# Optimization experiments

Measured on AMD Instinct MI355X. Metric: run time of the kernel, lower is better.

Reference implementation:

```python
import jax, jax.numpy as jnp
import numpy as np

B, C, H, W = 16, 64, 1024, 16  # requires C*W == H per the module's implicit view/matmul constraint
C8 = C // 8


def setup_inputs() -> dict:
    key = jax.random.key(0)
    ks = jax.random.split(key, 7)
    s_in = 1.0 / np.sqrt(C)
    return {
        "x": jax.random.normal(ks[0], (B, C, H, W), dtype=jnp.float32),
        "Wq": jax.random.normal(ks[1], (C8, C), dtype=jnp.float32) * s_in,
        "bq": jax.random.normal(ks[2], (C8,), dtype=jnp.float32) * 0.01,
        "Wk": jax.random.normal(ks[3], (C8, C), dtype=jnp.float32) * s_in,
        "bk": jax.random.normal(ks[4], (C8,), dtype=jnp.float32) * 0.01,
        "Wv": jax.random.normal(ks[5], (C, C), dtype=jnp.float32) * s_in,
        "bv": jax.random.normal(ks[6], (C,), dtype=jnp.float32) * 0.01,
    }


def conv1x1(x, w, b):
    # 1x1 conv == per-pixel channel mixing: [B,C,H,W] x [O,C] -> [B,O,H,W]
    return jnp.einsum("bchw,oc->bohw", x, w) + b[None, :, None, None]


def reference(x, Wq, bq, Wk, bk, Wv, bv):
    b, c, h, w = x.shape
    q = conv1x1(x, Wq, bq)  # [B, C/8, H, W]
    k = conv1x1(x, Wk, bk)  # [B, C/8, H, W]
    v = conv1x1(x, Wv, bv)  # [B, C, H, W]
    # Faithful to torch .view(B, -1, H): row-major reshape, NOT a transpose.
    qf = jnp.swapaxes(q.reshape(b, -1, h), 1, 2)  # [B, H, C8*W]
    kf = k.reshape(b, -1, h)                      # [B, C8*W, H]
    vf = v.reshape(b, -1, h)                      # [B, C*W, H] (C*W == H)
    scores = jax.nn.softmax(jnp.matmul(qf, kf), axis=-1)  # [B, H, H]
    attended = jnp.matmul(scores, vf)             # [B, H, H]
    attended = attended.reshape(v.shape)          # [B, C, H, W]
    return x + attended
```

## Files before the change

### kernel.cpp

```cpp
#include <hip/hip_runtime.h>
#include <stdint.h>

typedef uint32_t u32;
typedef __attribute__((ext_vector_type(4))) float f32x4;
typedef __attribute__((ext_vector_type(8))) short short8;

#define NBATCH 16
#define NPIX   16384
#define NPB    1048576

__device__ __forceinline__ ushort f2bf(float f) {
  u32 b = __builtin_bit_cast(u32, f);
  return (ushort)((b + 0x7FFFu + ((b >> 16) & 1u)) >> 16);
}
__device__ __forceinline__ float bf2f(ushort h) {
  return __builtin_bit_cast(float, (u32)h << 16);
}

__device__ __forceinline__ void gload16(const void* g, void* l) {
  __builtin_amdgcn_global_load_lds(
      (const __attribute__((address_space(1))) u32*)g,
      (__attribute__((address_space(3))) u32*)l,
      16, 0, 0);
}

__global__ void prep_w2(const float* __restrict__ Wq, const float* __restrict__ bq,
                        const float* __restrict__ Wk, const float* __restrict__ bk,
                        const float* __restrict__ Wv, const float* __restrict__ bv,
                        ushort* __restrict__ Wpk, float* __restrict__ bpk)
{
  int gid = blockIdx.x * 256 + threadIdx.x;
  if (gid < 12288) {
    int m = gid >> 7, kk = gid & 127;
    int ch = kk & 63;
    ushort outv = 0;
    if (m < 8) {
      float wv = Wq[m * 64 + ch];
      ushort h = f2bf(wv);
      outv = (kk < 64) ? h : f2bf(wv - bf2f(h));
    } else if (m < 16) {
      float wv = Wk[(m - 8) * 64 + ch];
      ushort h = f2bf(wv);
      outv = (kk < 64) ? h : f2bf(wv - bf2f(h));
    } else if (m < 80) {
      outv = (kk < 64) ? f2bf(Wv[(m - 16) * 64 + ch]) : (ushort)0;
    }
    Wpk[gid] = outv;
  } else if (gid < 12368) {
    int o = gid - 12288;
    bpk[o] = (o < 8) ? bq[o] : (o < 16 ? bk[o - 8] : bv[o - 16]);
  }
}

__global__ __launch_bounds__(256) void proj10(
    const float* __restrict__ x, const ushort* __restrict__ Wpk,
    const float* __restrict__ bpk,
    ushort* __restrict__ Qt2, ushort* __restrict__ Kt2,
    ushort* __restrict__ Vt)
{
  __shared__ __align__(16) char smem[32768];
  float* xs = (float*)smem;
  int t = threadIdx.x;
  int w = t >> 6, lane = t & 63;
  int l15 = lane & 15, l4 = lane >> 4;

  int g = blockIdx.x;
  int lin = (g & 7) * 256 + (g >> 3);
  int b = lin >> 7;
  int l0 = (lin & 127) << 3;
  const float* xb = x + (size_t)b * NPB + l0;

  #pragma unroll
  for (int it = 0; it < 8; ++it) {
    int f0 = (it * 4 + w) * 64;
    int f = f0 + lane;
    int ch = f >> 5, r2 = f & 31, tc = r2 >> 1, half = r2 & 1;
    gload16(xb + (size_t)ch * NPIX + tc * 1024 + half * 4, xs + f0 * 4);
  }

  const uint4* Wp4 = (const uint4*)Wpk;
  uint4 Afrag[12];
  #pragma unroll
  for (int kc = 0; kc < 4; ++kc)
    Afrag[kc] = Wp4[l15 * 16 + kc * 4 + l4];
  #pragma unroll
  for (int mt = 1; mt < 5; ++mt)
    #pragma unroll
    for (int kc = 0; kc < 2; ++kc)
      Afrag[2 + mt * 2 + kc] = Wp4[(mt * 16 + l15) * 16 + kc * 4 + l4];

  f32x4 acc[5][2];
  #pragma unroll
  for (int mt = 0; mt < 5; ++mt) {
    f32x4 bv4;
    #pragma unroll
    for (int r = 0; r < 4; ++r) bv4[r] = bpk[mt * 16 + l4 * 4 + r];
    acc[mt][0] = bv4; acc[mt][1] = bv4;
  }

  __syncthreads();

  #pragma unroll
  for (int i = 0; i < 2; ++i) {
    int px = (w * 2 + i) * 16 + l15;
    u32 xr[16];
    #pragma unroll
    for (int kc = 0; kc < 2; ++kc)
      #pragma unroll
      for (int j = 0; j < 8; ++j)
        xr[kc * 8 + j] = ((const u32*)xs)[(kc * 32 + l4 * 8 + j) * 128 + px];
    uint4 bxh[2], bxl[2];
    #pragma unroll
    for (int kc = 0; kc < 2; ++kc)
      #pragma unroll
      for (int p = 0; p < 4; ++p) {
        u32 a = xr[kc * 8 + 2 * p], c = xr[kc * 8 + 2 * p + 1];
        ((u32*)&bxh[kc])[p] = (a >> 16) | (c & 0xFFFF0000u);
        float fa = __builtin_bit_cast(float, a) -
                   __builtin_bit_cast(float, a & 0xFFFF0000u);
        float fc = __builtin_bit_cast(float, c) -
                   __builtin_bit_cast(float, c & 0xFFFF0000u);
        u32 la = __builtin_bit_cast(u32, fa), lc = __builtin_bit_cast(u32, fc);
        ((u32*)&bxl[kc])[p] = (la >> 16) | (lc & 0xFFFF0000u);
      }
    short8 h0 = __builtin_bit_cast(short8, bxh[0]);
    short8 h1 = __builtin_bit_cast(short8, bxh[1]);
    short8 s0 = __builtin_bit_cast(short8, bxl[0]);
    short8 s1 = __builtin_bit_cast(short8, bxl[1]);
    acc[0][i] = __builtin_amdgcn_mfma_f32_16x16x32_bf16(
        __builtin_bit_cast(short8, Afrag[0]), h0, acc[0][i], 0, 0, 0);
    acc[0][i] = __builtin_amdgcn_mfma_f32_16x16x32_bf16(
        __builtin_bit_cast(short8, Afrag[1]), h1, acc[0][i], 0, 0, 0);
    acc[0][i] = __builtin_amdgcn_mfma_f32_16x16x32_bf16(
        __builtin_bit_cast(short8, Afrag[0]), s0, acc[0][i], 0, 0, 0);
    acc[0][i] = __builtin_amdgcn_mfma_f32_16x16x32_bf16(
        __builtin_bit_cast(short8, Afrag[1]), s1, acc[0][i], 0, 0, 0);
    acc[0][i] = __builtin_amdgcn_mfma_f32_16x16x32_bf16(
        __builtin_bit_cast(short8, Afrag[2]), h0, acc[0][i], 0, 0, 0);
    acc[0][i] = __builtin_amdgcn_mfma_f32_16x16x32_bf16(
        __builtin_bit_cast(short8, Afrag[3]), h1, acc[0][i], 0, 0, 0);
    #pragma unroll
    for (int mt = 1; mt < 5; ++mt) {
      acc[mt][i] = __builtin_amdgcn_mfma_f32_16x16x32_bf16(
          __builtin_bit_cast(short8, Afrag[2 + mt * 2]), h0, acc[mt][i], 0, 0, 0);
      acc[mt][i] = __builtin_amdgcn_mfma_f32_16x16x32_bf16(
          __builtin_bit_cast(short8, Afrag[3 + mt * 2]), h1, acc[mt][i], 0, 0, 0);
    }
  }
  __syncthreads();

  float*  qkl = (float*)smem;
  ushort* vl  = (ushort*)(smem + 16 * 132 * 4);
  #pragma unroll
  for (int i = 0; i < 2; ++i) {
    int px = (w * 2 + i) * 16 + l15;
    #pragma unroll
    for (int r = 0; r < 4; ++r)
      qkl[(l4 * 4 + r) * 132 + px] = acc[0][i][r];
    #pragma unroll
    for (int mt = 1; mt < 5; ++mt)
      #pragma unroll
      for (int r = 0; r < 4; ++r)
        vl[((mt - 1) * 16 + l4 * 4 + r) * 136 + px] = f2bf(acc[mt][i][r]);
  }
  __syncthreads();

  if (t < 128) {
    int l = t >> 4, tcc = t & 15;
    size_t lrow = (size_t)b * 1024 + l0 + l;
    int px = tcc * 8 + l;

    union { ushort s[8]; uint4 v; } qh, ql, kh, kl;
    #pragma unroll
    for (int o = 0; o < 8; ++o) {
      float qv = qkl[o * 132 + px];
      ushort h = f2bf(qv);
      qh.s[o] = h; ql.s[o] = f2bf(qv - bf2f(h));
      float kv = qkl[(8 + o) * 132 + px];
      h = f2bf(kv);
      kh.s[o] = h; kl.s[o] = f2bf(kv - bf2f(h));
    }
    ushort* qrow = Qt2 + lrow * 384 + tcc * 8;
    *(uint4*)qrow         = qh.v;
    *(uint4*)(qrow + 128) = ql.v;
    *(uint4*)(qrow + 256) = qh.v;
    ushort* krow = Kt2 + lrow * 384 + tcc * 8;
    *(uint4*)krow         = kh.v;
    *(uint4*)(krow + 128) = kh.v;
    *(uint4*)(krow + 256) = kl.v;

    ushort* vrow = Vt + lrow * 1024;
    #pragma unroll
    for (int it = 0; it < 4; ++it) {
      int c2 = (it << 4) + tcc;
      union { ushort s[16]; uint4 q[2]; } ov;
      #pragma unroll
      for (int tt = 0; tt < 16; ++tt)
        ov.s[tt] = vl[c2 * 136 + tt * 8 + l];
      *(uint4*)(vrow + c2 * 16)     = ov.q[0];
      *(uint4*)(vrow + c2 * 16 + 8) = ov.q[1];
    }
  }
}

template<int KTOT, bool ADDX>
__global__ __launch_bounds__(512, 2) void gemm256(
    const ushort* __restrict__ A, int lda,
    const ushort* __restrict__ B, int ldb,
    float* __restrict__ C, const float* __restrict__ X)
{
  __shared__ ushort AB[2][2][16384];
  int t = threadIdx.x;

  int g = blockIdx.x;
  int lin = (g & 7) * 32 + (g >> 3);
  int bz = lin >> 4;
  int by = (lin >> 2) & 3;
  int bx = lin & 3;
  int m0 = by << 8, n0 = bx << 8;

  const ushort* Ab = A + (size_t)bz * 1024 * lda;
  const ushort* Bb = B + (size_t)bz * 1024 * ldb;
  int w = t >> 6, lane = t & 63;
  int wm = w >> 2, wn = w & 3;
  int l15 = lane & 15, l4 = lane >> 4;

  int swc = (t & 7) ^ ((t >> 3) & 7);
  const ushort* pa = Ab + (size_t)(m0 + (t >> 3)) * lda + swc * 8;
  const ushort* pb = Bb + (size_t)(n0 + (t >> 3)) * ldb + swc * 8;
  int wb = w * 512;

  f32x4 acc[8][4] = {};
  constexpr int NT = KTOT / 64;

  #pragma unroll
  for (int i = 0; i < 4; ++i)
    gload16(pa + (size_t)i * 64 * lda, AB[0][0] + i * 4096 + wb);
  #pragma unroll
  for (int i = 0; i < 4; ++i)
    gload16(pb + (size_t)i * 64 * ldb, AB[0][1] + i * 4096 + wb);
  #pragma unroll
  for (int i = 0; i < 4; ++i)
    gload16(pa + (size_t)i * 64 * lda + 64, AB[1][0] + i * 4096 + wb);
  #pragma unroll
  for (int i = 0; i < 4; ++i)
    gload16(pb + (size_t)i * 64 * ldb + 64, AB[1][1] + i * 4096 + wb);

  for (int it = 0; it < NT; ++it) {
    int cur = it & 1;
    asm volatile("s_waitcnt vmcnt(8)" ::: "memory");
    __builtin_amdgcn_sched_barrier(0);
    __builtin_amdgcn_s_barrier();

    const ushort* As = AB[cur][0];
    const ushort* Bs = AB[cur][1];
    #pragma unroll
    for (int kk = 0; kk < 2; ++kk) {
      short8 af[8], bfr[4];
      #pragma unroll
      for (int mi = 0; mi < 8; ++mi) {
        int rr = (wm << 7) + (mi << 4) + l15;
        af[mi] = __builtin_bit_cast(short8,
            ((const uint4*)As)[rr * 8 + ((kk * 4 + l4) ^ (rr & 7))]);
      }
      #pragma unroll
      for (int ni = 0; ni < 4; ++ni) {
        int rr = (wn << 6) + (ni << 4) + l15;
        bfr[ni] = __builtin_bit_cast(short8,
            ((const uint4*)Bs)[rr * 8 + ((kk * 4 + l4) ^ (rr & 7))]);
      }
      #pragma unroll
      for (int mi = 0; mi < 8; ++mi)
        #pragma unroll
        for (int ni = 0; ni < 4; ++ni)
          acc[mi][ni] = __builtin_amdgcn_mfma_f32_16x16x32_bf16(
              af[mi], bfr[ni], acc[mi][ni], 0, 0, 0);
    }

    asm volatile("" ::: "memory");
    __builtin_amdgcn_s_barrier();
    __builtin_amdgcn_sched_barrier(0);
    if (it + 2 < NT) {
      int k0 = (it + 2) * 64;
      ushort* An = AB[cur][0];
      ushort* Bn = AB[cur][1];
      #pragma unroll
      for (int i = 0; i < 4; ++i)
        gload16(pa + (size_t)i * 64 * lda + k0, An + i * 4096 + wb);
      #pragma unroll
      for (int i = 0; i < 4; ++i)
        gload16(pb + (size_t)i * 64 * ldb + k0, Bn + i * 4096 + wb);
    }
  }

  #pragma unroll
  for (int mi = 0; mi < 8; ++mi) {
    int rbase = m0 + (wm << 7) + (mi << 4) + (l4 << 2);
    #pragma unroll
    for (int ni = 0; ni < 4; ++ni) {
      int col = n0 + (wn << 6) + (ni << 4) + l15;
      f32x4 v = acc[mi][ni];
      #pragma unroll
      for (int rr = 0; rr < 4; ++rr) {
        size_t idx = ((size_t)bz * 1024 + rbase + rr) * 1024 + col;
        if (ADDX) C[idx] = v[rr] + X[idx];
        else      C[idx] = v[rr];
      }
    }
  }
}

__global__ __launch_bounds__(256) void softmax_rows(float* __restrict__ S)
{
  size_t rowi = blockIdx.x;
  float* srow = S + rowi * 1024;
  int t = threadIdx.x;
  float4 v = ((const float4*)srow)[t];
  float m = fmaxf(fmaxf(v.x, v.y), fmaxf(v.z, v.w));
  #pragma unroll
  for (int off = 32; off > 0; off >>= 1) m = fmaxf(m, __shfl_xor(m, off));
  __shared__ float red[8];
  int wid = t >> 6, lane = t & 63;
  if (lane == 0) red[wid] = m;
  __syncthreads();
  m = fmaxf(fmaxf(red[0], red[1]), fmaxf(red[2], red[3]));
  float e0 = __expf(v.x - m), e1 = __expf(v.y - m);
  float e2 = __expf(v.z - m), e3 = __expf(v.w - m);
  float s = e0 + e1 + e2 + e3;
  #pragma unroll
  for (int off = 32; off > 0; off >>= 1) s += __shfl_xor(s, off);
  if (lane == 0) red[4 + wid] = s;
  __syncthreads();
  s = red[4] + red[5] + red[6] + red[7];
  float inv = 1.0f / s;
  union { ushort h[4]; uint2 q; } pk;
  pk.h[0] = f2bf(e0 * inv); pk.h[1] = f2bf(e1 * inv);
  pk.h[2] = f2bf(e2 * inv); pk.h[3] = f2bf(e3 * inv);
  ((uint2*)srow)[t] = pk.q;
}

extern "C" void kernel_launch(void* const* d_in, const int* in_sizes, int n_in,
                              void* d_out, int out_size, void* d_ws, size_t ws_size,
                              hipStream_t stream) {
  const float* x  = (const float*)d_in[0];
  const float* Wq = (const float*)d_in[1];
  const float* bq = (const float*)d_in[2];
  const float* Wk = (const float*)d_in[3];
  const float* bk = (const float*)d_in[4];
  const float* Wv = (const float*)d_in[5];
  const float* bv = (const float*)d_in[6];
  float* out = (float*)d_out;

  char* wsb = (char*)d_ws;
  ushort* Qt2 = (ushort*)wsb;
  ushort* Kt2 = (ushort*)(wsb + 12582912);
  ushort* Vt  = (ushort*)(wsb + 25165824);
  float*  S   = (float*)(wsb + 58720256);
  ushort* Wpk = (ushort*)(wsb + 92274688);
  float*  bpk = (float*)(wsb + 92274688 + 24576);

  prep_w2<<<49, 256, 0, stream>>>(Wq, bq, Wk, bk, Wv, bv, Wpk, bpk);
  proj10<<<2048, 256, 0, stream>>>(x, Wpk, bpk, Qt2, Kt2, Vt);
  gemm256<384, false><<<256, 512, 0, stream>>>(Qt2, 384, Kt2, 384, S, nullptr);
  softmax_rows<<<16384, 256, 0, stream>>>(S);
  gemm256<1024, true><<<256, 512, 0, stream>>>((const ushort*)S, 2048, Vt, 1024, out, x);
}
```

Measured before the change: 126.5 us.

## Fuse row softmax into the attention-times-V GEMM prologue and A-tile loads

Removes the standalone softmax kernel and folds it into the second GEMM. Each block first scans its 256 score rows to get the row max and inverse sum. It then applies exp/normalize/bf16 conversion while staging the fp32 A tiles into shared memory. This avoids writing bf16 probabilities back to S and the separate launch. In exchange, each of the 4 column blocks redundantly reads fp32 S twice (stats pass plus tile pass) and recomputes exps, doubling A-side read bytes versus bf16.

```diff
diff --git a/kernel.cpp b/kernel.cpp
--- a/kernel.cpp
+++ b/kernel.cpp
@@ -310,33 +310,143 @@
   }
 }
 
-__global__ __launch_bounds__(256) void softmax_rows(float* __restrict__ S)
+__global__ __launch_bounds__(512, 2) void gemm256_sm(
+    const float* __restrict__ S,
+    const ushort* __restrict__ B, int ldb,
+    float* __restrict__ C, const float* __restrict__ X)
 {
-  size_t rowi = blockIdx.x;
-  float* srow = S + rowi * 1024;
+  __shared__ ushort Abuf[2][16384];
+  __shared__ ushort Bbuf[2][16384];
+  __shared__ float rowmax[256], rowinv[256];
   int t = threadIdx.x;
-  float4 v = ((const float4*)srow)[t];
-  float m = fmaxf(fmaxf(v.x, v.y), fmaxf(v.z, v.w));
-  #pragma unroll
-  for (int off = 32; off > 0; off >>= 1) m = fmaxf(m, __shfl_xor(m, off));
-  __shared__ float red[8];
-  int wid = t >> 6, lane = t & 63;
-  if (lane == 0) red[wid] = m;
+
+  int g = blockIdx.x;
+  int lin = (g & 7) * 32 + (g >> 3);
+  int bz = lin >> 4;
+  int by = (lin >> 2) & 3;
+  int bx = lin & 3;
+  int m0 = by << 8, n0 = bx << 8;
+
+  const float*  Sb = S + (size_t)bz * 1024 * 1024 + (size_t)m0 * 1024;
+  const ushort* Bb = B + (size_t)bz * 1024 * ldb;
+  int w = t >> 6, lane = t & 63;
+  int wm = w >> 2, wn = w & 3;
+  int l15 = lane & 15, l4 = lane >> 4;
+
+  for (int rr = 0; rr < 32; ++rr) {
+    int r = w * 32 + rr;
+    const float4* rp = (const float4*)(Sb + (size_t)r * 1024) + lane * 4;
+    float4 v0 = rp[0], v1 = rp[1], v2 = rp[2], v3 = rp[3];
+    float m = fmaxf(fmaxf(fmaxf(v0.x, v0.y), fmaxf(v0.z, v0.w)),
+                    fmaxf(fmaxf(v1.x, v1.y), fmaxf(v1.z, v1.w)));
+    m = fmaxf(m, fmaxf(fmaxf(fmaxf(v2.x, v2.y), fmaxf(v2.z, v2.w)),
+                       fmaxf(fmaxf(v3.x, v3.y), fmaxf(v3.z, v3.w))));
+    #pragma unroll
+    for (int off = 32; off > 0; off >>= 1) m = fmaxf(m, __shfl_xor(m, off));
+    float s = __expf(v0.x - m) + __expf(v0.y - m) + __expf(v0.z - m) + __expf(v0.w - m)
+            + __expf(v1.x - m) + __expf(v1.y - m) + __expf(v1.z - m) + __expf(v1.w - m)
+            + __expf(v2.x - m) + __expf(v2.y - m) + __expf(v2.z - m) + __expf(v2.w - m)
+            + __expf(v3.x - m) + __expf(v3.y - m) + __expf(v3.z - m) + __expf(v3.w - m);
+    #pragma unroll
+    for (int off = 32; off > 0; off >>= 1) s += __shfl_xor(s, off);
+    if (lane == 0) { rowmax[r] = m; rowinv[r] = 1.0f / s; }
+  }
   __syncthreads();
-  m = fmaxf(fmaxf(red[0], red[1]), fmaxf(red[2], red[3]));
-  float e0 = __expf(v.x - m), e1 = __expf(v.y - m);
-  float e2 = __expf(v.z - m), e3 = __expf(v.w - m);
-  float s = e0 + e1 + e2 + e3;
-  #pragma unroll
-  for (int off = 32; off > 0; off >>= 1) s += __shfl_xor(s, off);
-  if (lane == 0) red[4 + wid] = s;
+
+  int swc = (t & 7) ^ ((t >> 3) & 7);
+  const ushort* pb = Bb + (size_t)(n0 + (t >> 3)) * ldb + swc * 8;
+  int wb = w * 512;
+  int ci = t & 7, rb = t >> 3;
+
+  f32x4 acc[8][4] = {};
+  constexpr int NT = 16;
+  float4 sreg[4][2];
+
+  #define LOAD_A(k0_)                                                        \
+    _Pragma("unroll")                                                        \
+    for (int gi = 0; gi < 4; ++gi) {                                         \
+      const float* src = Sb + (size_t)(rb + 64 * gi) * 1024 + (k0_) + ci * 8;\
+      sreg[gi][0] = *(const float4*)src;                                     \
+      sreg[gi][1] = *(const float4*)(src + 4);                               \
+    }
+  #define WRITE_A(dst_)                                                      \
+    _Pragma("unroll")                                                        \
+    for (int gi = 0; gi < 4; ++gi) {                                         \
+      int r = rb + 64 * gi;                                                  \
+      float mx = rowmax[r], iv = rowinv[r];                                  \
+      union { ushort s[8]; uint4 q; } pk;                                    \
+      _Pragma("unroll")                                                      \
+      for (int j = 0; j < 4; ++j) {                                          \
+        pk.s[j]     = f2bf(__expf(((const float*)&sreg[gi][0])[j] - mx) * iv);\
+        pk.s[4 + j] = f2bf(__expf(((const float*)&sreg[gi][1])[j] - mx) * iv);\
+      }                                                                      \
+      ((uint4*)(dst_))[r * 8 + (ci ^ (r & 7))] = pk.q;                       \
+    }
+
+  LOAD_A(0)
+  #pragma unroll
+  for (int i = 0; i < 4; ++i)
+    gload16(pb + (size_t)i * 64 * ldb, Bbuf[0] + i * 4096 + wb);
+  asm volatile("s_waitcnt vmcnt(0)" ::: "memory");
+  WRITE_A(Abuf[0])
   __syncthreads();
-  s = red[4] + red[5] + red[6] + red[7];
-  float inv = 1.0f / s;
-  union { ushort h[4]; uint2 q; } pk;
-  pk.h[0] = f2bf(e0 * inv); pk.h[1] = f2bf(e1 * inv);
-  pk.h[2] = f2bf(e2 * inv); pk.h[3] = f2bf(e3 * inv);
-  ((uint2*)srow)[t] = pk.q;
+
+  for (int it = 0; it < NT; ++it) {
+    int cur = it & 1;
+    if (it + 1 < NT) {
+      LOAD_A((it + 1) * 64)
+      #pragma unroll
+      for (int i = 0; i < 4; ++i)
+        gload16(pb + (size_t)i * 64 * ldb + (it + 1) * 64,
+                Bbuf[cur ^ 1] + i * 4096 + wb);
+    }
+    const ushort* As = Abuf[cur];
+    const ushort* Bs = Bbuf[cur];
+    #pragma unroll
+    for (int kk = 0; kk < 2; ++kk) {
+      short8 af[8], bfr[4];
+      #pragma unroll
+      for (int mi = 0; mi < 8; ++mi) {
+        int rr = (wm << 7) + (mi << 4) + l15;
+        af[mi] = __builtin_bit_cast(short8,
+            ((const uint4*)As)[rr * 8 + ((kk * 4 + l4) ^ (rr & 7))]);
+      }
+      #pragma unroll
+      for (int ni = 0; ni < 4; ++ni) {
+        int rr = (wn << 6) + (ni << 4) + l15;
+        bfr[ni] = __builtin_bit_cast(short8,
+            ((const uint4*)Bs)[rr * 8 + ((kk * 4 + l4) ^ (rr & 7))]);
+      }
+      #pragma unroll
+      for (int mi = 0; mi < 8; ++mi)
+        #pragma unroll
+        for (int ni = 0; ni < 4; ++ni)
+          acc[mi][ni] = __builtin_amdgcn_mfma_f32_16x16x32_bf16(
+              af[mi], bfr[ni], acc[mi][ni], 0, 0, 0);
+    }
+    asm volatile("s_waitcnt vmcnt(0)" ::: "memory");
+    if (it + 1 < NT) {
+      WRITE_A(Abuf[cur ^ 1])
+    }
+    __syncthreads();
+  }
+
+  #pragma unroll
+  for (int mi = 0; mi < 8; ++mi) {
+    int rbase = m0 + (wm << 7) + (mi << 4) + (l4 << 2);
+    #pragma unroll
+    for (int ni = 0; ni < 4; ++ni) {
+      int col = n0 + (wn << 6) + (ni << 4) + l15;
+      f32x4 v = acc[mi][ni];
+      #pragma unroll
+      for (int rr = 0; rr < 4; ++rr) {
+        size_t idx = ((size_t)bz * 1024 + rbase + rr) * 1024 + col;
+        C[idx] = v[rr] + X[idx];
+      }
+    }
+  }
+  #undef LOAD_A
+  #undef WRITE_A
 }
 
 extern "C" void kernel_launch(void* const* d_in, const int* in_sizes, int n_in,
@@ -362,6 +472,5 @@
   prep_w2<<<49, 256, 0, stream>>>(Wq, bq, Wk, bk, Wv, bv, Wpk, bpk);
   proj10<<<2048, 256, 0, stream>>>(x, Wpk, bpk, Qt2, Kt2, Vt);
   gemm256<384, false><<<256, 512, 0, stream>>>(Qt2, 384, Kt2, 384, S, nullptr);
-  softmax_rows<<<16384, 256, 0, stream>>>(S);
-  gemm256<1024, true><<<256, 512, 0, stream>>>((const ushort*)S, 2048, Vt, 1024, out, x);
-}
+  gemm256_sm<<<256, 512, 0, stream>>>(S, Vt, 1024, out, x);
+}
```

Result: slower. 151.8 us (+20.0%).

## Shrink Q/K split-bf16 storage and double-buffer x loads in projection

Applied to the files above, without the earlier changes.

Q and K are now stored as hi/lo pairs (256 columns) instead of the duplicated three-segment 384-column layout. A dedicated QK GEMM iterates over the three needed cross-term pairs (hh, lh, hl) via index tables. This cuts Q/K write and read traffic by a third. The projection kernel now processes two 8-row chunks per block, issuing both chunks' x loads up front so the second chunk's load overlaps the first chunk's compute. The cost is twice the shared memory per block and therefore possibly lower occupancy.

```diff
diff --git a/kernel.cpp b/kernel.cpp
--- a/kernel.cpp
+++ b/kernel.cpp
@@ -52,31 +52,21 @@
   }
 }
 
-__global__ __launch_bounds__(256) void proj10(
+__global__ __launch_bounds__(256) void proj12(
     const float* __restrict__ x, const ushort* __restrict__ Wpk,
     const float* __restrict__ bpk,
     ushort* __restrict__ Qt2, ushort* __restrict__ Kt2,
     ushort* __restrict__ Vt)
 {
-  __shared__ __align__(16) char smem[32768];
-  float* xs = (float*)smem;
+  __shared__ __align__(16) char smem[65536];
   int t = threadIdx.x;
   int w = t >> 6, lane = t & 63;
   int l15 = lane & 15, l4 = lane >> 4;
 
   int g = blockIdx.x;
-  int lin = (g & 7) * 256 + (g >> 3);
-  int b = lin >> 7;
-  int l0 = (lin & 127) << 3;
-  const float* xb = x + (size_t)b * NPB + l0;
-
-  #pragma unroll
-  for (int it = 0; it < 8; ++it) {
-    int f0 = (it * 4 + w) * 64;
-    int f = f0 + lane;
-    int ch = f >> 5, r2 = f & 31, tc = r2 >> 1, half = r2 & 1;
-    gload16(xb + (size_t)ch * NPIX + tc * 1024 + half * 4, xs + f0 * 4);
-  }
+  int lin = (g & 7) * 128 + (g >> 3);
+  int b = lin >> 6;
+  int l0 = (lin & 63) << 4;
 
   const uint4* Wp4 = (const uint4*)Wpk;
   uint4 Afrag[12];
@@ -88,117 +78,241 @@
     #pragma unroll
     for (int kc = 0; kc < 2; ++kc)
       Afrag[2 + mt * 2 + kc] = Wp4[(mt * 16 + l15) * 16 + kc * 4 + l4];
-
-  f32x4 acc[5][2];
-  #pragma unroll
-  for (int mt = 0; mt < 5; ++mt) {
-    f32x4 bv4;
-    #pragma unroll
-    for (int r = 0; r < 4; ++r) bv4[r] = bpk[mt * 16 + l4 * 4 + r];
-    acc[mt][0] = bv4; acc[mt][1] = bv4;
-  }
-
-  __syncthreads();
-
-  #pragma unroll
-  for (int i = 0; i < 2; ++i) {
-    int px = (w * 2 + i) * 16 + l15;
-    u32 xr[16];
-    #pragma unroll
-    for (int kc = 0; kc < 2; ++kc)
-      #pragma unroll
-      for (int j = 0; j < 8; ++j)
-        xr[kc * 8 + j] = ((const u32*)xs)[(kc * 32 + l4 * 8 + j) * 128 + px];
-    uint4 bxh[2], bxl[2];
-    #pragma unroll
-    for (int kc = 0; kc < 2; ++kc)
-      #pragma unroll
-      for (int p = 0; p < 4; ++p) {
-        u32 a = xr[kc * 8 + 2 * p], c = xr[kc * 8 + 2 * p + 1];
-        ((u32*)&bxh[kc])[p] = (a >> 16) | (c & 0xFFFF0000u);
-        float fa = __builtin_bit_cast(float, a) -
-                   __builtin_bit_cast(float, a & 0xFFFF0000u);
-        float fc = __builtin_bit_cast(float, c) -
-                   __builtin_bit_cast(float, c & 0xFFFF0000u);
-        u32 la = __builtin_bit_cast(u32, fa), lc = __builtin_bit_cast(u32, fc);
-        ((u32*)&bxl[kc])[p] = (la >> 16) | (lc & 0xFFFF0000u);
-      }
-    short8 h0 = __builtin_bit_cast(short8, bxh[0]);
-    short8 h1 = __builtin_bit_cast(short8, bxh[1]);
-    short8 s0 = __builtin_bit_cast(short8, bxl[0]);
-    short8 s1 = __builtin_bit_cast(short8, bxl[1]);
-    acc[0][i] = __builtin_amdgcn_mfma_f32_16x16x32_bf16(
-        __builtin_bit_cast(short8, Afrag[0]), h0, acc[0][i], 0, 0, 0);
-    acc[0][i] = __builtin_amdgcn_mfma_f32_16x16x32_bf16(
-        __builtin_bit_cast(short8, Afrag[1]), h1, acc[0][i], 0, 0, 0);
-    acc[0][i] = __builtin_amdgcn_mfma_f32_16x16x32_bf16(
-        __builtin_bit_cast(short8, Afrag[0]), s0, acc[0][i], 0, 0, 0);
-    acc[0][i] = __builtin_amdgcn_mfma_f32_16x16x32_bf16(
-        __builtin_bit_cast(short8, Afrag[1]), s1, acc[0][i], 0, 0, 0);
-    acc[0][i] = __builtin_amdgcn_mfma_f32_16x16x32_bf16(
-        __builtin_bit_cast(short8, Afrag[2]), h0, acc[0][i], 0, 0, 0);
-    acc[0][i] = __builtin_amdgcn_mfma_f32_16x16x32_bf16(
-        __builtin_bit_cast(short8, Afrag[3]), h1, acc[0][i], 0, 0, 0);
-    #pragma unroll
-    for (int mt = 1; mt < 5; ++mt) {
-      acc[mt][i] = __builtin_amdgcn_mfma_f32_16x16x32_bf16(
-          __builtin_bit_cast(short8, Afrag[2 + mt * 2]), h0, acc[mt][i], 0, 0, 0);
-      acc[mt][i] = __builtin_amdgcn_mfma_f32_16x16x32_bf16(
-          __builtin_bit_cast(short8, Afrag[3 + mt * 2]), h1, acc[mt][i], 0, 0, 0);
-    }
-  }
-  __syncthreads();
-
-  float*  qkl = (float*)smem;
-  ushort* vl  = (ushort*)(smem + 16 * 132 * 4);
-  #pragma unroll
-  for (int i = 0; i < 2; ++i) {
-    int px = (w * 2 + i) * 16 + l15;
-    #pragma unroll
-    for (int r = 0; r < 4; ++r)
-      qkl[(l4 * 4 + r) * 132 + px] = acc[0][i][r];
-    #pragma unroll
-    for (int mt = 1; mt < 5; ++mt)
+  __builtin_amdgcn_sched_barrier(0);
+
+  #pragma unroll
+  for (int c = 0; c < 2; ++c) {
+    const float* xb = x + (size_t)b * NPB + l0 + c * 8;
+    float* xs = (float*)(smem + c * 32768);
+    #pragma unroll
+    for (int it = 0; it < 8; ++it) {
+      int f0 = (it * 4 + w) * 64;
+      int f = f0 + lane;
+      int ch = f >> 5, r2 = f & 31, tc = r2 >> 1, half = r2 & 1;
+      gload16(xb + (size_t)ch * NPIX + tc * 1024 + half * 4, xs + f0 * 4);
+    }
+  }
+  asm volatile("s_waitcnt vmcnt(8)" ::: "memory");
+  __builtin_amdgcn_sched_barrier(0);
+  __builtin_amdgcn_s_barrier();
+
+  auto do_chunk = [&](char* region, int lc) {
+    float* xs = (float*)region;
+    f32x4 acc[5][2];
+    #pragma unroll
+    for (int mt = 0; mt < 5; ++mt) {
+      f32x4 bv4;
+      #pragma unroll
+      for (int r = 0; r < 4; ++r) bv4[r] = bpk[mt * 16 + l4 * 4 + r];
+      acc[mt][0] = bv4; acc[mt][1] = bv4;
+    }
+    #pragma unroll
+    for (int i = 0; i < 2; ++i) {
+      int px = (w * 2 + i) * 16 + l15;
+      u32 xr[16];
+      #pragma unroll
+      for (int kc = 0; kc < 2; ++kc)
+        #pragma unroll
+        for (int j = 0; j < 8; ++j)
+          xr[kc * 8 + j] = ((const u32*)xs)[(kc * 32 + l4 * 8 + j) * 128 + px];
+      uint4 bxh[2], bxl[2];
+      #pragma unroll
+      for (int kc = 0; kc < 2; ++kc)
+        #pragma unroll
+        for (int p = 0; p < 4; ++p) {
+          u32 a = xr[kc * 8 + 2 * p], cc = xr[kc * 8 + 2 * p + 1];
+          ((u32*)&bxh[kc])[p] = (a >> 16) | (cc & 0xFFFF0000u);
+          float fa = __builtin_bit_cast(float, a) -
+                     __builtin_bit_cast(float, a & 0xFFFF0000u);
+          float fc = __builtin_bit_cast(float, cc) -
+                     __builtin_bit_cast(float, cc & 0xFFFF0000u);
+          u32 la = __builtin_bit_cast(u32, fa), lc2 = __builtin_bit_cast(u32, fc);
+          ((u32*)&bxl[kc])[p] = (la >> 16) | (lc2 & 0xFFFF0000u);
+        }
+      short8 h0 = __builtin_bit_cast(short8, bxh[0]);
+      short8 h1 = __builtin_bit_cast(short8, bxh[1]);
+      short8 s0 = __builtin_bit_cast(short8, bxl[0]);
+      short8 s1 = __builtin_bit_cast(short8, bxl[1]);
+      acc[0][i] = __builtin_amdgcn_mfma_f32_16x16x32_bf16(
+          __builtin_bit_cast(short8, Afrag[0]), h0, acc[0][i], 0, 0, 0);
+      acc[0][i] = __builtin_amdgcn_mfma_f32_16x16x32_bf16(
+          __builtin_bit_cast(short8, Afrag[1]), h1, acc[0][i], 0, 0, 0);
+      acc[0][i] = __builtin_amdgcn_mfma_f32_16x16x32_bf16(
+          __builtin_bit_cast(short8, Afrag[0]), s0, acc[0][i], 0, 0, 0);
+      acc[0][i] = __builtin_amdgcn_mfma_f32_16x16x32_bf16(
+          __builtin_bit_cast(short8, Afrag[1]), s1, acc[0][i], 0, 0, 0);
+      acc[0][i] = __builtin_amdgcn_mfma_f32_16x16x32_bf16(
+          __builtin_bit_cast(short8, Afrag[2]), h0, acc[0][i], 0, 0, 0);
+      acc[0][i] = __builtin_amdgcn_mfma_f32_16x16x32_bf16(
+          __builtin_bit_cast(short8, Afrag[3]), h1, acc[0][i], 0, 0, 0);
+      #pragma unroll
+      for (int mt = 1; mt < 5; ++mt) {
+        acc[mt][i] = __builtin_amdgcn_mfma_f32_16x16x32_bf16(
+            __builtin_bit_cast(short8, Afrag[2 + mt * 2]), h0, acc[mt][i], 0, 0, 0);
+        acc[mt][i] = __builtin_amdgcn_mfma_f32_16x16x32_bf16(
+            __builtin_bit_cast(short8, Afrag[3 + mt * 2]), h1, acc[mt][i], 0, 0, 0);
+      }
+    }
+    __syncthreads();
+
+    float*  qkl = (float*)region;
+    ushort* vl  = (ushort*)(region + 16 * 132 * 4);
+    #pragma unroll
+    for (int i = 0; i < 2; ++i) {
+      int px = (w * 2 + i) * 16 + l15;
       #pragma unroll
       for (int r = 0; r < 4; ++r)
-        vl[((mt - 1) * 16 + l4 * 4 + r) * 136 + px] = f2bf(acc[mt][i][r]);
-  }
-  __syncthreads();
-
-  if (t < 128) {
-    int l = t >> 4, tcc = t & 15;
-    size_t lrow = (size_t)b * 1024 + l0 + l;
-    int px = tcc * 8 + l;
-
-    union { ushort s[8]; uint4 v; } qh, ql, kh, kl;
-    #pragma unroll
-    for (int o = 0; o < 8; ++o) {
-      float qv = qkl[o * 132 + px];
-      ushort h = f2bf(qv);
-      qh.s[o] = h; ql.s[o] = f2bf(qv - bf2f(h));
-      float kv = qkl[(8 + o) * 132 + px];
-      h = f2bf(kv);
-      kh.s[o] = h; kl.s[o] = f2bf(kv - bf2f(h));
-    }
-    ushort* qrow = Qt2 + lrow * 384 + tcc * 8;
-    *(uint4*)qrow         = qh.v;
-    *(uint4*)(qrow + 128) = ql.v;
-    *(uint4*)(qrow + 256) = qh.v;
-    ushort* krow = Kt2 + lrow * 384 + tcc * 8;
-    *(uint4*)krow         = kh.v;
-    *(uint4*)(krow + 128) = kh.v;
-    *(uint4*)(krow + 256) = kl.v;
-
-    ushort* vrow = Vt + lrow * 1024;
-    #pragma unroll
-    for (int it = 0; it < 4; ++it) {
-      int c2 = (it << 4) + tcc;
-      union { ushort s[16]; uint4 q[2]; } ov;
-      #pragma unroll
-      for (int tt = 0; tt < 16; ++tt)
-        ov.s[tt] = vl[c2 * 136 + tt * 8 + l];
-      *(uint4*)(vrow + c2 * 16)     = ov.q[0];
-      *(uint4*)(vrow + c2 * 16 + 8) = ov.q[1];
+        qkl[(l4 * 4 + r) * 132 + px] = acc[0][i][r];
+      #pragma unroll
+      for (int mt = 1; mt < 5; ++mt)
+        #pragma unroll
+        for (int r = 0; r < 4; ++r)
+          vl[((mt - 1) * 16 + l4 * 4 + r) * 136 + px] = f2bf(acc[mt][i][r]);
+    }
+    __syncthreads();
+
+    if (t < 128) {
+      int l = t >> 4, tcc = t & 15;
+      size_t lrow = (size_t)b * 1024 + lc + l;
+      int px = tcc * 8 + l;
+
+      union { ushort s[8]; uint4 v; } qh, ql, kh, kl;
+      #pragma unroll
+      for (int o = 0; o < 8; ++o) {
+        float qv = qkl[o * 132 + px];
+        ushort h = f2bf(qv);
+        qh.s[o] = h; ql.s[o] = f2bf(qv - bf2f(h));
+        float kv = qkl[(8 + o) * 132 + px];
+        h = f2bf(kv);
+        kh.s[o] = h; kl.s[o] = f2bf(kv - bf2f(h));
+      }
+      ushort* qrow = Qt2 + lrow * 256 + tcc * 8;
+      *(uint4*)qrow         = qh.v;
+      *(uint4*)(qrow + 128) = ql.v;
+      ushort* krow = Kt2 + lrow * 256 + tcc * 8;
+      *(uint4*)krow         = kh.v;
+      *(uint4*)(krow + 128) = kl.v;
+
+      ushort* vrow = Vt + lrow * 1024;
+      #pragma unroll
+      for (int it = 0; it < 4; ++it) {
+        int c2 = (it << 4) + tcc;
+        union { ushort s[16]; uint4 q[2]; } ov;
+        #pragma unroll
+        for (int tt = 0; tt < 16; ++tt)
+          ov.s[tt] = vl[c2 * 136 + tt * 8 + l];
+        *(uint4*)(vrow + c2 * 16)     = ov.q[0];
+        *(uint4*)(vrow + c2 * 16 + 8) = ov.q[1];
+      }
+    }
+  };
+
+  do_chunk(smem, l0);
+  do_chunk(smem + 32768, l0 + 8);
+}
+
+__global__ __launch_bounds__(512, 2) void gemm_qk(
+    const ushort* __restrict__ A,
+    const ushort* __restrict__ B,
+    float* __restrict__ C)
+{
+  __shared__ ushort AB[2][2][16384];
+  int t = threadIdx.x;
+
+  int g = blockIdx.x;
+  int lin = (g & 7) * 32 + (g >> 3);
+  int bz = lin >> 4;
+  int by = (lin >> 2) & 3;
+  int bx = lin & 3;
+  int m0 = by << 8, n0 = bx << 8;
+
+  const ushort* Ab = A + (size_t)bz * 1024 * 256;
+  const ushort* Bb = B + (size_t)bz * 1024 * 256;
+  int w = t >> 6, lane = t & 63;
+  int wm = w >> 2, wn = w & 3;
+  int l15 = lane & 15, l4 = lane >> 4;
+
+  int swc = (t & 7) ^ ((t >> 3) & 7);
+  const ushort* pa = Ab + (size_t)(m0 + (t >> 3)) * 256 + swc * 8;
+  const ushort* pb = Bb + (size_t)(n0 + (t >> 3)) * 256 + swc * 8;
+  int wb = w * 512;
+
+  constexpr int KA[6] = {0, 64, 128, 192, 0, 64};
+  constexpr int KB[6] = {0, 64, 0, 64, 128, 192};
+
+  f32x4 acc[8][4] = {};
+
+  #pragma unroll
+  for (int i = 0; i < 4; ++i)
+    gload16(pa + (size_t)i * 64 * 256 + KA[0], AB[0][0] + i * 4096 + wb);
+  #pragma unroll
+  for (int i = 0; i < 4; ++i)
+    gload16(pb + (size_t)i * 64 * 256 + KB[0], AB[0][1] + i * 4096 + wb);
+  #pragma unroll
+  for (int i = 0; i < 4; ++i)
+    gload16(pa + (size_t)i * 64 * 256 + KA[1], AB[1][0] + i * 4096 + wb);
+  #pragma unroll
+  for (int i = 0; i < 4; ++i)
+    gload16(pb + (size_t)i * 64 * 256 + KB[1], AB[1][1] + i * 4096 + wb);
+
+  for (int it = 0; it < 6; ++it) {
+    int cur = it & 1;
+    asm volatile("s_waitcnt vmcnt(8)" ::: "memory");
+    __builtin_amdgcn_sched_barrier(0);
+    __builtin_amdgcn_s_barrier();
+
+    const ushort* As = AB[cur][0];
+    const ushort* Bs = AB[cur][1];
+    #pragma unroll
+    for (int kk = 0; kk < 2; ++kk) {
+      short8 af[8], bfr[4];
+      #pragma unroll
+      for (int mi = 0; mi < 8; ++mi) {
+        int rr = (wm << 7) + (mi << 4) + l15;
+        af[mi] = __builtin_bit_cast(short8,
+            ((const uint4*)As)[rr * 8 + ((kk * 4 + l4) ^ (rr & 7))]);
+      }
+      #pragma unroll
+      for (int ni = 0; ni < 4; ++ni) {
+        int rr = (wn << 6) + (ni << 4) + l15;
+        bfr[ni] = __builtin_bit_cast(short8,
+            ((const uint4*)Bs)[rr * 8 + ((kk * 4 + l4) ^ (rr & 7))]);
+      }
+      #pragma unroll
+      for (int mi = 0; mi < 8; ++mi)
+        #pragma unroll
+        for (int ni = 0; ni < 4; ++ni)
+          acc[mi][ni] = __builtin_amdgcn_mfma_f32_16x16x32_bf16(
+              af[mi], bfr[ni], acc[mi][ni], 0, 0, 0);
+    }
+
+    asm volatile("" ::: "memory");
+    __builtin_amdgcn_s_barrier();
+    __builtin_amdgcn_sched_barrier(0);
+    if (it + 2 < 6) {
+      ushort* An = AB[cur][0];
+      ushort* Bn = AB[cur][1];
+      #pragma unroll
+      for (int i = 0; i < 4; ++i)
+        gload16(pa + (size_t)i * 64 * 256 + KA[it + 2], An + i * 4096 + wb);
+      #pragma unroll
+      for (int i = 0; i < 4; ++i)
+        gload16(pb + (size_t)i * 64 * 256 + KB[it + 2], Bn + i * 4096 + wb);
+    }
+  }
+
+  #pragma unroll
+  for (int mi = 0; mi < 8; ++mi) {
+    int rbase = m0 + (wm << 7) + (mi << 4) + (l4 << 2);
+    #pragma unroll
+    for (int ni = 0; ni < 4; ++ni) {
+      int col = n0 + (wn << 6) + (ni << 4) + l15;
+      f32x4 v = acc[mi][ni];
+      #pragma unroll
+      for (int rr = 0; rr < 4; ++rr) {
+        size_t idx = ((size_t)bz * 1024 + rbase + rr) * 1024 + col;
+        C[idx] = v[rr];
+      }
     }
   }
 }
@@ -353,15 +467,15 @@
 
   char* wsb = (char*)d_ws;
   ushort* Qt2 = (ushort*)wsb;
-  ushort* Kt2 = (ushort*)(wsb + 12582912);
-  ushort* Vt  = (ushort*)(wsb + 25165824);
-  float*  S   = (float*)(wsb + 58720256);
-  ushort* Wpk = (ushort*)(wsb + 92274688);
-  float*  bpk = (float*)(wsb + 92274688 + 24576);
+  ushort* Kt2 = (ushort*)(wsb + 8388608);
+  ushort* Vt  = (ushort*)(wsb + 16777216);
+  float*  S   = (float*)(wsb + 50331648);
+  ushort* Wpk = (ushort*)(wsb + 117440512);
+  float*  bpk = (float*)(wsb + 117440512 + 24576);
 
   prep_w2<<<49, 256, 0, stream>>>(Wq, bq, Wk, bk, Wv, bv, Wpk, bpk);
-  proj10<<<2048, 256, 0, stream>>>(x, Wpk, bpk, Qt2, Kt2, Vt);
-  gemm256<384, false><<<256, 512, 0, stream>>>(Qt2, 384, Kt2, 384, S, nullptr);
+  proj12<<<1024, 256, 0, stream>>>(x, Wpk, bpk, Qt2, Kt2, Vt);
+  gemm_qk<<<256, 512, 0, stream>>>(Qt2, Kt2, S);
   softmax_rows<<<16384, 256, 0, stream>>>(S);
   gemm256<1024, true><<<256, 512, 0, stream>>>((const ushort*)S, 2048, Vt, 1024, out, x);
 }
```

Measured after the change: 124.0 us. -2.0%, faster.
